# Kernel optimization log

Measured on AMD Instinct MI355X. Metric: run time of the kernel, lower is better.

Reference implementation:

```python
import jax, jax.numpy as jnp
import numpy as np

SPLINE_ORDER = 3


def _bsplines(x, grid, k=SPLINE_ORDER):
    # x: [..., ]  grid: [G] (uniform, shared across in-features)
    # returns Cox-de Boor bases of order k: [..., G-1-k]
    x = x[..., None]
    bases = ((x >= grid[:-1]) & (x < grid[1:])).astype(x.dtype)
    for j in range(1, k + 1):
        left = (x - grid[: -(j + 1)]) / (grid[j:-1] - grid[: -(j + 1)]) * bases[..., :-1]
        right = (grid[j + 1:] - x) / (grid[j + 1:] - grid[1:-j]) * bases[..., 1:]
        bases = left + right
    return bases


def _kan_conv(x, base_w, spline_w, scaler, grid):
    # x: [B, C, H, W]; applies 5 independent KANLinear(9 -> 1) over 3x3 patches
    B, C, H, W = x.shape
    Ho, Wo = H - 2, W - 2
    patches = jax.lax.conv_general_dilated_patches(x, (3, 3), (1, 1), 'VALID')  # [B, C*9, Ho, Wo] (channel-major)
    p = patches.reshape(B, C, 9, Ho, Wo).transpose(0, 1, 3, 4, 2)  # [B, C, Ho, Wo, 9]
    sw = spline_w * scaler[..., None]  # [K, 9, S]
    sb = _bsplines(p, grid)            # [B, C, Ho, Wo, 9, S]
    out = (jnp.einsum('bchwi,ki->bchwk', jax.nn.silu(p), base_w)
           + jnp.einsum('bchwis,kis->bchwk', sb, sw))  # [B, C, Ho, Wo, K]
    # channel layout: for each input channel, the K conv outputs (c*K + k)
    return out.transpose(0, 1, 4, 2, 3).reshape(B, C * base_w.shape[0], Ho, Wo)


def _maxpool2(x):
    B, C, H, W = x.shape
    H2, W2 = H // 2, W // 2
    return x[:, :, :H2 * 2, :W2 * 2].reshape(B, C, H2, 2, W2, 2).max(axis=(3, 5))


def _forward(x, conv1_base, conv1_spline, conv1_scaler,
             conv2_base, conv2_spline, conv2_scaler,
             kan1_base, kan1_spline, kan1_scaler):
    dt = x.dtype
    # extended uniform grids (grid_range extended by spline_order*h on each side)
    grid1 = (jnp.arange(-3, 5 + 3 + 1, dtype=dt) * (2.0 / 5) - 1.0)    # grid_size=5,  range [-1,1], 12 pts
    grid2 = (jnp.arange(-3, 10 + 3 + 1, dtype=dt) * (2.0 / 10) - 1.0)  # grid_size=10, range [-1,1], 17 pts
    grid3 = (jnp.arange(-3, 10 + 3 + 1, dtype=dt) * (1.0 / 10))        # grid_size=10, range [0,1],  17 pts

    h = _kan_conv(x, conv1_base, conv1_spline, conv1_scaler, grid1)  # [B,5,26,26]
    h = _maxpool2(h)                                                  # [B,5,13,13]
    h = _kan_conv(h, conv2_base, conv2_spline, conv2_scaler, grid2)  # [B,25,11,11]
    h = _maxpool2(h)                                                  # [B,25,5,5]
    B = h.shape[0]
    f = h.reshape(B, -1)                                              # [B,625]

    sw = kan1_spline * kan1_scaler[..., None]                         # [10,625,13]
    sb = _bsplines(f, grid3)                                          # [B,625,13]
    logits = jax.nn.silu(f) @ kan1_base.T + jnp.einsum('bis,ois->bo', sb, sw)
    return jax.nn.log_softmax(logits, axis=1)


def setup_inputs() -> dict:
    key = jax.random.key(0)
    ks = jax.random.split(key, 10)
    d = jnp.float32
    return {
        'x': jax.random.uniform(ks[0], (1024, 1, 28, 28), dtype=d),
        'conv1_base': jax.random.normal(ks[1], (5, 9), dtype=d) * 0.3,
        'conv1_spline': jax.random.normal(ks[2], (5, 9, 8), dtype=d) * 0.1,
        'conv1_scaler': jax.random.normal(ks[3], (5, 9), dtype=d) * 0.3 + 1.0,
        'conv2_base': jax.random.normal(ks[4], (5, 9), dtype=d) * 0.3,
        'conv2_spline': jax.random.normal(ks[5], (5, 9, 13), dtype=d) * 0.1,
        'conv2_scaler': jax.random.normal(ks[6], (5, 9), dtype=d) * 0.3 + 1.0,
        'kan1_base': jax.random.normal(ks[7], (10, 625), dtype=d) * 0.05,
        'kan1_spline': jax.random.normal(ks[8], (10, 625, 13), dtype=d) * 0.05,
        'kan1_scaler': jax.random.normal(ks[9], (10, 625), dtype=d) * 0.3 + 1.0,
    }


def reference(x, conv1_base, conv1_spline, conv1_scaler,
              conv2_base, conv2_spline, conv2_scaler,
              kan1_base, kan1_spline, kan1_scaler):
    return _forward(x, conv1_base, conv1_spline, conv1_scaler,
                    conv2_base, conv2_spline, conv2_scaler,
                    kan1_base, kan1_spline, kan1_scaler)
```

## Files before the change

### kernel.cpp

```cpp
#include <hip/hip_runtime.h>

#define DEV __device__ __forceinline__

DEV float silu_f(float v) { return v / (1.0f + __expf(-v)); }

DEV int bspline4(float x, float g0, float inv_h, int imax, float w[4]) {
  float t = (x - g0) * inv_h;
  float fi = floorf(t);
  int i = (int)fi;
  if (t < 0.0f || i > imax) { w[0] = w[1] = w[2] = w[3] = 0.0f; return 0; }
  float u = t - fi;
  float u2 = u * u, u3 = u2 * u;
  float om = 1.0f - u;
  const float c6 = 1.0f / 6.0f;
  w[0] = om * om * om * c6;
  w[1] = (3.0f * u3 - 6.0f * u2 + 4.0f) * c6;
  w[2] = (-3.0f * u3 + 3.0f * u2 + 3.0f * u + 1.0f) * c6;
  w[3] = u3 * c6;
  return i - 3;
}

DEV float4 cubic_coeffs(float s0, float s1, float s2, float s3) {
  float4 c;
  const float c6 = 1.0f / 6.0f;
  c.x = (s0 + 4.0f * s1 + s2) * c6;
  c.y = (s2 - s0) * 0.5f;
  c.z = (s0 - 2.0f * s1 + s2) * 0.5f;
  c.w = (s3 - s0 + 3.0f * (s1 - s2)) * c6;
  return c;
}

__global__ __launch_bounds__(512, 6) void kkan_fused(
    const float* __restrict__ x,
    const float* __restrict__ c1b, const float* __restrict__ c1s, const float* __restrict__ c1sc,
    const float* __restrict__ c2b, const float* __restrict__ c2s, const float* __restrict__ c2sc,
    const float* __restrict__ kb,  const float* __restrict__ ks,  const float* __restrict__ ksc,
    float* __restrict__ out)
{
  __shared__ float  xs[784];
  __shared__ float4 tab1[9 * 5 * 12];
  __shared__ float4 tab2[9 * 5 * 17];
  __shared__ float  w1b[45];
  __shared__ float  w2b[45];
  __shared__ float  h1p[5 * 13 * 13];
  __shared__ float  fv[625];
  __shared__ float  lred[8][10];
  __shared__ float  lfin[10];

  const int b = blockIdx.x;
  const int tid = threadIdx.x;

  const float* xb = x + b * 784;
  for (int i = tid; i < 784; i += 512) xs[i] = xb[i];
  for (int i = tid; i < 45; i += 512) { w1b[i] = c1b[i]; w2b[i] = c2b[i]; }
  #pragma unroll 1
  for (int idx = tid; idx < 540; idx += 512) {
    const int tap = idx / 60, rem = idx % 60;
    const int k = rem / 12, iv = rem % 12;
    float4 c = make_float4(0.f, 0.f, 0.f, 0.f);
    if (iv <= 10) {
      const float sc = c1sc[k * 9 + tap];
      const float* sw = &c1s[(k * 9 + tap) * 8];
      float s[4];
      #pragma unroll
      for (int j = 0; j < 4; ++j) {
        const int m = iv - 3 + j;
        s[j] = ((unsigned)m < 8u) ? sw[m] * sc : 0.f;
      }
      c = cubic_coeffs(s[0], s[1], s[2], s[3]);
    }
    tab1[idx] = c;
  }
  #pragma unroll 1
  for (int idx = tid; idx < 765; idx += 512) {
    const int tap = idx / 85, rem = idx % 85;
    const int k = rem / 17, iv = rem % 17;
    float4 c = make_float4(0.f, 0.f, 0.f, 0.f);
    if (iv <= 15) {
      const float sc = c2sc[k * 9 + tap];
      const float* sw = &c2s[(k * 9 + tap) * 13];
      float s[4];
      #pragma unroll
      for (int j = 0; j < 4; ++j) {
        const int m = iv - 3 + j;
        s[j] = ((unsigned)m < 13u) ? sw[m] * sc : 0.f;
      }
      c = cubic_coeffs(s[0], s[1], s[2], s[3]);
    }
    tab2[idx] = c;
  }
  __syncthreads();

  #pragma unroll 1
  for (int q = tid; q < 676; q += 512) {
    const int pos = q >> 2, quad = q & 3;
    const int pi = pos / 13, pj = pos % 13;
    const int oh = 2 * pi + (quad >> 1), ow = 2 * pj + (quad & 1);
    float acc[5] = {0.f, 0.f, 0.f, 0.f, 0.f};
    #pragma unroll 1
    for (int kh = 0; kh < 3; ++kh) {
      #pragma unroll 1
      for (int kw = 0; kw < 3; ++kw) {
        const int tap = kh * 3 + kw;
        const float v = xs[(oh + kh) * 28 + (ow + kw)];
        const float sil = silu_f(v);
        const float t = (v + 2.2f) * 2.5f;
        const float fi = floorf(t);
        const int i = (int)fi;
        const int ic = ((unsigned)i <= 10u) ? i : 11;
        const float u = t - fi;
        const float4* tp = &tab1[tap * 60 + ic];
        #pragma unroll
        for (int k = 0; k < 5; ++k) {
          const float4 c = tp[k * 12];
          const float sp = ((c.w * u + c.z) * u + c.y) * u + c.x;
          acc[k] += sil * w1b[k * 9 + tap] + sp;
        }
      }
    }
    #pragma unroll
    for (int k = 0; k < 5; ++k) {
      float m = acc[k];
      m = fmaxf(m, __shfl_xor(m, 1));
      m = fmaxf(m, __shfl_xor(m, 2));
      if (quad == 0) h1p[(k * 13 + pi) * 13 + pj] = m;
    }
  }
  __syncthreads();

  if (tid < 500) {
    const int pos = tid >> 2, quad = tid & 3;
    const int c = pos / 25, rr = pos % 25;
    const int y = rr / 5, xx = rr % 5;
    const int oh = 2 * y + (quad >> 1), ow = 2 * xx + (quad & 1);
    float acc[5] = {0.f, 0.f, 0.f, 0.f, 0.f};
    #pragma unroll 1
    for (int kh = 0; kh < 3; ++kh) {
      #pragma unroll 1
      for (int kw = 0; kw < 3; ++kw) {
        const int tap = kh * 3 + kw;
        const float v = h1p[(c * 13 + oh + kh) * 13 + (ow + kw)];
        const float sil = silu_f(v);
        const float t = (v + 1.6f) * 5.0f;
        const float fi = floorf(t);
        const int i = (int)fi;
        const int ic = ((unsigned)i <= 15u) ? i : 16;
        const float u = t - fi;
        const float4* tp = &tab2[tap * 85 + ic];
        #pragma unroll
        for (int k = 0; k < 5; ++k) {
          const float4 cc = tp[k * 17];
          const float sp = ((cc.w * u + cc.z) * u + cc.y) * u + cc.x;
          acc[k] += sil * w2b[k * 9 + tap] + sp;
        }
      }
    }
    #pragma unroll
    for (int k = 0; k < 5; ++k) {
      float m = acc[k];
      m = fmaxf(m, __shfl_xor(m, 1));
      m = fmaxf(m, __shfl_xor(m, 2));
      if (quad == 0) fv[(c * 5 + k) * 25 + rr] = m;
    }
  }
  __syncthreads();

  float acc[10] = {0.f, 0.f, 0.f, 0.f, 0.f, 0.f, 0.f, 0.f, 0.f, 0.f};
  #pragma unroll 1
  for (int i = tid; i < 625; i += 512) {
    const float v = fv[i];
    const float sil = silu_f(v);
    float w[4];
    const int m0 = bspline4(v, -0.3f, 10.0f, 15, w);
    int idx[4];
    #pragma unroll
    for (int j = 0; j < 4; ++j) {
      const int m = m0 + j;
      const bool ok = ((unsigned)m < 13u);
      idx[j] = ok ? m : 0;
      w[j] = ok ? w[j] : 0.f;
    }
    #pragma unroll 2
    for (int o = 0; o < 10; ++o) {
      const int wi = o * 625 + i;
      const float* sp = ks + (size_t)wi * 13;
      const float s = w[0] * sp[idx[0]] + w[1] * sp[idx[1]]
                    + w[2] * sp[idx[2]] + w[3] * sp[idx[3]];
      acc[o] += sil * kb[wi] + s * ksc[wi];
    }
  }
  #pragma unroll
  for (int o = 0; o < 10; ++o) {
    float v = acc[o];
    for (int off = 32; off > 0; off >>= 1) v += __shfl_down(v, off);
    acc[o] = v;
  }
  const int wave = tid >> 6, lane = tid & 63;
  if (lane == 0) {
    #pragma unroll
    for (int o = 0; o < 10; ++o) lred[wave][o] = acc[o];
  }
  __syncthreads();
  if (tid < 10) {
    float s = 0.f;
    #pragma unroll
    for (int wv = 0; wv < 8; ++wv) s += lred[wv][tid];
    lfin[tid] = s;
  }
  __syncthreads();
  if (tid == 0) {
    float mx = lfin[0];
    #pragma unroll
    for (int o = 1; o < 10; ++o) mx = fmaxf(mx, lfin[o]);
    float s = 0.f;
    #pragma unroll
    for (int o = 0; o < 10; ++o) s += __expf(lfin[o] - mx);
    const float ls = logf(s) + mx;
    #pragma unroll
    for (int o = 0; o < 10; ++o) out[b * 10 + o] = lfin[o] - ls;
  }
}

extern "C" void kernel_launch(void* const* d_in, const int* in_sizes, int n_in,
                              void* d_out, int out_size, void* d_ws, size_t ws_size,
                              hipStream_t stream) {
  (void)n_in; (void)d_ws; (void)ws_size; (void)out_size;
  const float* x    = (const float*)d_in[0];
  const float* c1b  = (const float*)d_in[1];
  const float* c1s  = (const float*)d_in[2];
  const float* c1sc = (const float*)d_in[3];
  const float* c2b  = (const float*)d_in[4];
  const float* c2s  = (const float*)d_in[5];
  const float* c2sc = (const float*)d_in[6];
  const float* kb   = (const float*)d_in[7];
  const float* ks   = (const float*)d_in[8];
  const float* ksc  = (const float*)d_in[9];
  float* out = (float*)d_out;

  const int B = in_sizes[0] / 784;
  kkan_fused<<<dim3(B), dim3(512), 0, stream>>>(
      x, c1b, c1s, c1sc, c2b, c2s, c2sc, kb, ks, ksc, out);
}
```

Measured before the change: 40.53 us.

## Precompute per-pixel silu and spline index once, share table buffer across stages

Each input pixel's silu value, fractional offset and clamped knot index are computed once into a shared-memory array. Previously they were recomputed for every one of the 9 taps that read that pixel. The same is done for the pooled stage-1 output before stage 2. The stage-1 and stage-2 spline tables share one buffer, with stage 2's table built after stage 1 finishes, and occupancy hints rise from 6 to 8 blocks. This costs an extra barrier pass and float4 LDS reads in exchange for less transcendental and floor work.

```diff
diff --git a/kernel.cpp b/kernel.cpp
--- a/kernel.cpp
+++ b/kernel.cpp
@@ -30,19 +30,18 @@
   return c;
 }
 
-__global__ __launch_bounds__(512, 6) void kkan_fused(
+__global__ __launch_bounds__(512, 8) void kkan_fused(
     const float* __restrict__ x,
     const float* __restrict__ c1b, const float* __restrict__ c1s, const float* __restrict__ c1sc,
     const float* __restrict__ c2b, const float* __restrict__ c2s, const float* __restrict__ c2sc,
     const float* __restrict__ kb,  const float* __restrict__ ks,  const float* __restrict__ ksc,
     float* __restrict__ out)
 {
-  __shared__ float  xs[784];
-  __shared__ float4 tab1[9 * 5 * 12];
-  __shared__ float4 tab2[9 * 5 * 17];
+  __shared__ float4 tabU[765];
+  __shared__ float4 pre[845];
   __shared__ float  w1b[45];
   __shared__ float  w2b[45];
-  __shared__ float  h1p[5 * 13 * 13];
+  __shared__ float  h1p[845];
   __shared__ float  fv[625];
   __shared__ float  lred[8][10];
   __shared__ float  lfin[10];
@@ -50,8 +49,21 @@
   const int b = blockIdx.x;
   const int tid = threadIdx.x;
 
-  const float* xb = x + b * 784;
-  for (int i = tid; i < 784; i += 512) xs[i] = xb[i];
+  const float4* xb4 = (const float4*)(x + b * 784);
+  #pragma unroll 1
+  for (int i = tid; i < 196; i += 512) {
+    const float4 v4 = xb4[i];
+    const float vs[4] = {v4.x, v4.y, v4.z, v4.w};
+    #pragma unroll
+    for (int j = 0; j < 4; ++j) {
+      const float v = vs[j];
+      const float t = (v + 2.2f) * 2.5f;
+      const float fi = floorf(t);
+      int ic = (int)fi;
+      ic = ((unsigned)ic <= 10u) ? ic : 11;
+      pre[i * 4 + j] = make_float4(silu_f(v), t - fi, __int_as_float(ic), 0.f);
+    }
+  }
   for (int i = tid; i < 45; i += 512) { w1b[i] = c1b[i]; w2b[i] = c2b[i]; }
   #pragma unroll 1
   for (int idx = tid; idx < 540; idx += 512) {
@@ -69,8 +81,43 @@
       }
       c = cubic_coeffs(s[0], s[1], s[2], s[3]);
     }
-    tab1[idx] = c;
-  }
+    tabU[idx] = c;
+  }
+  __syncthreads();
+
+  #pragma unroll 1
+  for (int q = tid; q < 676; q += 512) {
+    const int pos = q >> 2, quad = q & 3;
+    const int pi = pos / 13, pj = pos % 13;
+    const int oh = 2 * pi + (quad >> 1), ow = 2 * pj + (quad & 1);
+    float acc[5] = {0.f, 0.f, 0.f, 0.f, 0.f};
+    #pragma unroll 1
+    for (int kh = 0; kh < 3; ++kh) {
+      #pragma unroll 1
+      for (int kw = 0; kw < 3; ++kw) {
+        const int tap = kh * 3 + kw;
+        const float4 pc = pre[(oh + kh) * 28 + (ow + kw)];
+        const float sil = pc.x, u = pc.y;
+        const int ic = __float_as_int(pc.z);
+        const float4* tp = &tabU[tap * 60 + ic];
+        #pragma unroll
+        for (int k = 0; k < 5; ++k) {
+          const float4 c = tp[k * 12];
+          const float sp = ((c.w * u + c.z) * u + c.y) * u + c.x;
+          acc[k] += sil * w1b[k * 9 + tap] + sp;
+        }
+      }
+    }
+    #pragma unroll
+    for (int k = 0; k < 5; ++k) {
+      float m = acc[k];
+      m = fmaxf(m, __shfl_xor(m, 1));
+      m = fmaxf(m, __shfl_xor(m, 2));
+      if (quad == 0) h1p[(k * 13 + pi) * 13 + pj] = m;
+    }
+  }
+  __syncthreads();
+
   #pragma unroll 1
   for (int idx = tid; idx < 765; idx += 512) {
     const int tap = idx / 85, rem = idx % 85;
@@ -87,44 +134,16 @@
       }
       c = cubic_coeffs(s[0], s[1], s[2], s[3]);
     }
-    tab2[idx] = c;
-  }
-  __syncthreads();
-
-  #pragma unroll 1
-  for (int q = tid; q < 676; q += 512) {
-    const int pos = q >> 2, quad = q & 3;
-    const int pi = pos / 13, pj = pos % 13;
-    const int oh = 2 * pi + (quad >> 1), ow = 2 * pj + (quad & 1);
-    float acc[5] = {0.f, 0.f, 0.f, 0.f, 0.f};
-    #pragma unroll 1
-    for (int kh = 0; kh < 3; ++kh) {
-      #pragma unroll 1
-      for (int kw = 0; kw < 3; ++kw) {
-        const int tap = kh * 3 + kw;
-        const float v = xs[(oh + kh) * 28 + (ow + kw)];
-        const float sil = silu_f(v);
-        const float t = (v + 2.2f) * 2.5f;
-        const float fi = floorf(t);
-        const int i = (int)fi;
-        const int ic = ((unsigned)i <= 10u) ? i : 11;
-        const float u = t - fi;
-        const float4* tp = &tab1[tap * 60 + ic];
-        #pragma unroll
-        for (int k = 0; k < 5; ++k) {
-          const float4 c = tp[k * 12];
-          const float sp = ((c.w * u + c.z) * u + c.y) * u + c.x;
-          acc[k] += sil * w1b[k * 9 + tap] + sp;
-        }
-      }
-    }
-    #pragma unroll
-    for (int k = 0; k < 5; ++k) {
-      float m = acc[k];
-      m = fmaxf(m, __shfl_xor(m, 1));
-      m = fmaxf(m, __shfl_xor(m, 2));
-      if (quad == 0) h1p[(k * 13 + pi) * 13 + pj] = m;
-    }
+    tabU[idx] = c;
+  }
+  #pragma unroll 1
+  for (int i = tid; i < 845; i += 512) {
+    const float v = h1p[i];
+    const float t = (v + 1.6f) * 5.0f;
+    const float fi = floorf(t);
+    int ic = (int)fi;
+    ic = ((unsigned)ic <= 15u) ? ic : 16;
+    pre[i] = make_float4(silu_f(v), t - fi, __int_as_float(ic), 0.f);
   }
   __syncthreads();
 
@@ -139,14 +158,10 @@
       #pragma unroll 1
       for (int kw = 0; kw < 3; ++kw) {
         const int tap = kh * 3 + kw;
-        const float v = h1p[(c * 13 + oh + kh) * 13 + (ow + kw)];
-        const float sil = silu_f(v);
-        const float t = (v + 1.6f) * 5.0f;
-        const float fi = floorf(t);
-        const int i = (int)fi;
-        const int ic = ((unsigned)i <= 15u) ? i : 16;
-        const float u = t - fi;
-        const float4* tp = &tab2[tap * 85 + ic];
+        const float4 pc = pre[(c * 13 + oh + kh) * 13 + (ow + kw)];
+        const float sil = pc.x, u = pc.y;
+        const int ic = __float_as_int(pc.z);
+        const float4* tp = &tabU[tap * 85 + ic];
         #pragma unroll
         for (int k = 0; k < 5; ++k) {
           const float4 cc = tp[k * 17];
```

After: 45.48 us. 1.12x slower.
